# Optimization experiments

Measured on AMD Instinct MI355X. Metric: run time of the kernel, lower is better.

The kernel has to match this reference:

```python
import jax, jax.numpy as jnp
import numpy as np

B, T, D_MODEL, HEAD = 8, 2048, 1024, 64
NEG = -1e9  # finite mask fill; exp underflows to 0 in softmax, avoids inf/NaN


def setup_inputs() -> dict:
    key = jax.random.key(0)
    k1, k2, k3, k4, k5 = jax.random.split(key, 5)
    x = jax.random.normal(k1, (B, T, D_MODEL), dtype=jnp.float32)
    valid_lens = jax.random.randint(k2, (B,), 0, T)
    # nn.Linear(d_model, head_size, bias=False): y = x @ W, W: (d_model, head_size)
    s = 0.02
    Wq = jax.random.normal(k3, (D_MODEL, HEAD), dtype=jnp.float32) * s
    Wk = jax.random.normal(k4, (D_MODEL, HEAD), dtype=jnp.float32) * s
    Wv = jax.random.normal(k5, (D_MODEL, HEAD), dtype=jnp.float32) * s
    return {"x": x, "Wq": Wq, "Wk": Wk, "Wv": Wv, "valid_lens": valid_lens}


def reference(x, Wq, Wk, Wv, valid_lens):
    # x: (B, T, D), projections -> (B, T, H)
    q = jnp.einsum("btd,dh->bth", x, Wq)
    k = jnp.einsum("btd,dh->bth", x, Wk)
    v = jnp.einsum("btd,dh->bth", x, Wv)
    scale = k.shape[-1] ** -0.5
    wei = jnp.einsum("bqh,bkh->bqk", q, k) * scale  # (B, T, T)

    t = jnp.arange(T)
    causal = t[None, :] <= t[:, None]                     # (T, T) lower-tri
    valid = t[None, :] < valid_lens[:, None]              # (B, T)
    mask = causal[None, :, :] & valid[:, :, None] & valid[:, None, :]  # (B, T, T)

    wei = jnp.where(mask, wei, NEG)
    attn = jax.nn.softmax(wei, axis=2)
    # rows with no valid key get all-masked scores -> original code zeros them out
    row_all_masked = ~jnp.any(mask, axis=2)               # (B, T)
    attn = jnp.where(row_all_masked[:, :, None], 0.0, attn)
    # dropout(p=0.0) == identity
    out = jnp.einsum("bqk,bkh->bqh", attn, v)             # (B, T, H)
    return out
```

## Files before the change

kernel.cpp:

```cpp
#include <hip/hip_runtime.h>
#include <hip/hip_bf16.h>
#include <stdint.h>

#define T_   2048
#define DM_  1024
#define HD_  64
#define NROW 16384

typedef __attribute__((ext_vector_type(8))) __bf16 bf16x8;
typedef __attribute__((ext_vector_type(4))) __bf16 bf16x4;
typedef __attribute__((ext_vector_type(4))) float  f32x4;

__global__ void wconv_k(const float* __restrict__ Wq, const float* __restrict__ Wk,
                        const float* __restrict__ Wv, __bf16* __restrict__ wfrag) {
    int tid  = blockIdx.x * 256 + threadIdx.x;
    int lane = tid & 63;
    int t    = (tid >> 6) % 12;
    int kc   = tid / (12 * 64);
    int c = lane & 15, g = lane >> 4;
    int n = t * 16 + c;
    const float* W = (n < 64) ? Wq : (n < 128) ? Wk : Wv;
    int col = n & 63;
    int k0  = kc * 32 + g * 8;
    __bf16* dst = wfrag + (size_t)tid * 8;
#pragma unroll
    for (int j = 0; j < 8; ++j) dst[j] = (__bf16)W[(k0 + j) * HD_ + col];
}

__global__ __launch_bounds__(256) void proj_k(const float* __restrict__ x,
        const __bf16* __restrict__ wfrag, __bf16* __restrict__ Qb,
        __bf16* __restrict__ Kb, __bf16* __restrict__ Vt) {
    int lane = threadIdx.x & 63, wave = threadIdx.x >> 6;
    int ng = blockIdx.x >> 8;
    int rt = blockIdx.x & 255;
    int c = lane & 15, g = lane >> 4;
    int row0 = rt * 64 + wave * 16;
    const float* xp = x + (size_t)(row0 + c) * DM_ + g * 8;
    f32x4 acc[4];
#pragma unroll
    for (int t = 0; t < 4; ++t) acc[t] = (f32x4)0.f;
    for (int kc = 0; kc < 32; ++kc) {
        const f32x4* ap = (const f32x4*)(xp + kc * 32);
        f32x4 a0 = ap[0], a1 = ap[1];
        bf16x8 af;
#pragma unroll
        for (int j = 0; j < 4; ++j) { af[j] = (__bf16)a0[j]; af[j + 4] = (__bf16)a1[j]; }
        const bf16x8* bp = (const bf16x8*)(wfrag + (size_t)kc * 12 * 512) + ng * 256;
#pragma unroll
        for (int t = 0; t < 4; ++t) {
            bf16x8 bf = bp[t * 64 + lane];
            acc[t] = __builtin_amdgcn_mfma_f32_16x16x32_bf16(af, bf, acc[t], 0, 0, 0);
        }
    }
#pragma unroll
    for (int t = 0; t < 4; ++t) {
        int ncol = t * 16 + c;
#pragma unroll
        for (int r = 0; r < 4; ++r) {
            int grow = row0 + g * 4 + r;
            float v  = acc[t][r];
            if (ng == 0)      Qb[(size_t)grow * HD_ + ncol] = (__bf16)(v * 0.125f);
            else if (ng == 1) Kb[(size_t)grow * HD_ + ncol] = (__bf16)v;
            else              Vt[(size_t)(grow >> 11) * (HD_ * T_) + (size_t)ncol * T_ + (grow & 2047)] = (__bf16)v;
        }
    }
}

__global__ __launch_bounds__(128) void attn_k(const __bf16* __restrict__ Qb,
        const __bf16* __restrict__ Kb, const __bf16* __restrict__ Vt,
        const int* __restrict__ vlen, float* __restrict__ out) {
    int bid  = blockIdx.x;
    int half = bid >> 8, idx = bid & 255;
    int b = idx >> 5, p = idx & 31;
    int qb = half ? (63 - p) : p;
    int wave = threadIdx.x >> 6, lane = threadIdx.x & 63;
    int c = lane & 15, g = lane >> 4;
    int qg = qb * 32 + wave * 16 + c;
    const __bf16* qp = Qb + (size_t)(b * T_ + qg) * HD_ + g * 8;
    bf16x8 qf0 = *(const bf16x8*)qp;
    bf16x8 qf1 = *(const bf16x8*)(qp + 32);
    const __bf16* Kbase = Kb + (size_t)b * T_ * HD_;
    const __bf16* Vbase = Vt + (size_t)b * HD_ * T_;
    f32x4 o0 = (f32x4)0.f, o1 = (f32x4)0.f, o2 = (f32x4)0.f, o3 = (f32x4)0.f;
    float m = -1e30f, lsum = 0.f;
    __shared__ __bf16 plds[2][16][72];
    __bf16 (*pl)[72] = plds[wave];
    int nd2 = (qb + 2) >> 1;
    for (int kt = 0; kt < nd2; ++kt) {
        int kv0 = kt * 64;
        const __bf16* kp = Kbase + (size_t)(kv0 + c) * HD_ + g * 8;
        bf16x8 ka00 = *(const bf16x8*)(kp);
        bf16x8 ka01 = *(const bf16x8*)(kp + 32);
        bf16x8 ka10 = *(const bf16x8*)(kp + 16 * HD_);
        bf16x8 ka11 = *(const bf16x8*)(kp + 16 * HD_ + 32);
        bf16x8 kb00 = *(const bf16x8*)(kp + 32 * HD_);
        bf16x8 kb01 = *(const bf16x8*)(kp + 32 * HD_ + 32);
        bf16x8 kb10 = *(const bf16x8*)(kp + 48 * HD_);
        bf16x8 kb11 = *(const bf16x8*)(kp + 48 * HD_ + 32);
        f32x4 sa0 = (f32x4)0.f, sa1 = (f32x4)0.f, sb0 = (f32x4)0.f, sb1 = (f32x4)0.f;
        sa0 = __builtin_amdgcn_mfma_f32_16x16x32_bf16(ka00, qf0, sa0, 0, 0, 0);
        sa0 = __builtin_amdgcn_mfma_f32_16x16x32_bf16(ka01, qf1, sa0, 0, 0, 0);
        sa1 = __builtin_amdgcn_mfma_f32_16x16x32_bf16(ka10, qf0, sa1, 0, 0, 0);
        sa1 = __builtin_amdgcn_mfma_f32_16x16x32_bf16(ka11, qf1, sa1, 0, 0, 0);
        sb0 = __builtin_amdgcn_mfma_f32_16x16x32_bf16(kb00, qf0, sb0, 0, 0, 0);
        sb0 = __builtin_amdgcn_mfma_f32_16x16x32_bf16(kb01, qf1, sb0, 0, 0, 0);
        sb1 = __builtin_amdgcn_mfma_f32_16x16x32_bf16(kb10, qf0, sb1, 0, 0, 0);
        sb1 = __builtin_amdgcn_mfma_f32_16x16x32_bf16(kb11, qf1, sb1, 0, 0, 0);
        float s[16];
#pragma unroll
        for (int r = 0; r < 4; ++r) {
            s[r] = sa0[r]; s[4 + r] = sa1[r]; s[8 + r] = sb0[r]; s[12 + r] = sb1[r];
        }
        if (kt == nd2 - 1) {
#pragma unroll
            for (int i = 0; i < 16; ++i) {
                int kv = kv0 + (i >> 2) * 16 + g * 4 + (i & 3);
                if (kv > qg) s[i] = -1e30f;
            }
        }
        float tm = s[0];
#pragma unroll
        for (int i = 1; i < 16; ++i) tm = fmaxf(tm, s[i]);
        tm = fmaxf(tm, __shfl_xor(tm, 16));
        tm = fmaxf(tm, __shfl_xor(tm, 32));
        float mn = fmaxf(m, tm);
        float al = __expf(m - mn);
        float ps = 0.f;
#pragma unroll
        for (int i = 0; i < 16; ++i) { s[i] = __expf(s[i] - mn); ps += s[i]; }
        ps += __shfl_xor(ps, 16);
        ps += __shfl_xor(ps, 32);
        lsum = lsum * al + ps;
        m = mn;
        o0 *= al; o1 *= al; o2 *= al; o3 *= al;
#pragma unroll
        for (int mt = 0; mt < 4; ++mt) {
            bf16x4 pv;
#pragma unroll
            for (int r = 0; r < 4; ++r) pv[r] = (__bf16)s[mt * 4 + r];
            *(bf16x4*)&pl[c][mt * 16 + g * 4] = pv;
        }
        bf16x8 pf0 = *(const bf16x8*)&pl[c][g * 8];
        bf16x8 pf1 = *(const bf16x8*)&pl[c][32 + g * 8];
        const __bf16* vp = Vbase + (size_t)c * T_ + kv0 + g * 8;
        bf16x8 v0a = *(const bf16x8*)(vp);
        bf16x8 v1a = *(const bf16x8*)(vp + 16 * T_);
        bf16x8 v2a = *(const bf16x8*)(vp + 32 * T_);
        bf16x8 v3a = *(const bf16x8*)(vp + 48 * T_);
        bf16x8 v0b = *(const bf16x8*)(vp + 32);
        bf16x8 v1b = *(const bf16x8*)(vp + 16 * T_ + 32);
        bf16x8 v2b = *(const bf16x8*)(vp + 32 * T_ + 32);
        bf16x8 v3b = *(const bf16x8*)(vp + 48 * T_ + 32);
        o0 = __builtin_amdgcn_mfma_f32_16x16x32_bf16(v0a, pf0, o0, 0, 0, 0);
        o1 = __builtin_amdgcn_mfma_f32_16x16x32_bf16(v1a, pf0, o1, 0, 0, 0);
        o2 = __builtin_amdgcn_mfma_f32_16x16x32_bf16(v2a, pf0, o2, 0, 0, 0);
        o3 = __builtin_amdgcn_mfma_f32_16x16x32_bf16(v3a, pf0, o3, 0, 0, 0);
        o0 = __builtin_amdgcn_mfma_f32_16x16x32_bf16(v0b, pf1, o0, 0, 0, 0);
        o1 = __builtin_amdgcn_mfma_f32_16x16x32_bf16(v1b, pf1, o1, 0, 0, 0);
        o2 = __builtin_amdgcn_mfma_f32_16x16x32_bf16(v2b, pf1, o2, 0, 0, 0);
        o3 = __builtin_amdgcn_mfma_f32_16x16x32_bf16(v3b, pf1, o3, 0, 0, 0);
    }
    float inv  = 1.f / lsum;
    bool  dead = (qg >= vlen[b]);
    float* op  = out + (size_t)(b * T_ + qg) * HD_ + g * 4;
    f32x4 r0 = dead ? (f32x4)0.f : o0 * inv;
    f32x4 r1 = dead ? (f32x4)0.f : o1 * inv;
    f32x4 r2 = dead ? (f32x4)0.f : o2 * inv;
    f32x4 r3 = dead ? (f32x4)0.f : o3 * inv;
    *(f32x4*)(op)      = r0;
    *(f32x4*)(op + 16) = r1;
    *(f32x4*)(op + 32) = r2;
    *(f32x4*)(op + 48) = r3;
}

extern "C" void kernel_launch(void* const* d_in, const int* in_sizes, int n_in,
                              void* d_out, int out_size, void* d_ws, size_t ws_size,
                              hipStream_t stream) {
    const float* x   = (const float*)d_in[0];
    const float* Wq  = (const float*)d_in[1];
    const float* Wk  = (const float*)d_in[2];
    const float* Wv  = (const float*)d_in[3];
    const int*   vln = (const int*)d_in[4];
    float* out = (float*)d_out;

    __bf16* Qb    = (__bf16*)d_ws;
    __bf16* Kb    = Qb + (size_t)NROW * HD_;
    __bf16* Vt    = Kb + (size_t)NROW * HD_;
    __bf16* wfrag = Vt + (size_t)NROW * HD_;

    wconv_k<<<96, 256, 0, stream>>>(Wq, Wk, Wv, wfrag);
    proj_k <<<768, 256, 0, stream>>>(x, wfrag, Qb, Kb, Vt);
    attn_k <<<512, 128, 0, stream>>>(Qb, Kb, Vt, vln, out);
}
```

Baseline: 175.4 us.

## Split attention KV loop four ways and merge partials in a combine kernel

Splits each query tile's causal KV loop into four interleaved partitions run by separate blocks. Each block writes unnormalised partial outputs plus running max and sum to workspace, and a new combine kernel merges them with log-sum-exp rescaling and applies the valid-length zeroing. This raises block count to increase GPU occupancy and parallelism. The softmax also switches to exp2 by folding log2(e) into the Q scale. It adds a second launch and extra float partial traffic through global memory.

```diff
diff --git a/kernel.cpp b/kernel.cpp
--- a/kernel.cpp
+++ b/kernel.cpp
@@ -6,6 +6,7 @@
 #define DM_  1024
 #define HD_  64
 #define NROW 16384
+#define SPLIT 4
 
 typedef __attribute__((ext_vector_type(8))) __bf16 bf16x8;
 typedef __attribute__((ext_vector_type(4))) __bf16 bf16x4;
@@ -59,7 +60,7 @@
         for (int r = 0; r < 4; ++r) {
             int grow = row0 + g * 4 + r;
             float v  = acc[t][r];
-            if (ng == 0)      Qb[(size_t)grow * HD_ + ncol] = (__bf16)(v * 0.125f);
+            if (ng == 0)      Qb[(size_t)grow * HD_ + ncol] = (__bf16)(v * 0.18033688f);
             else if (ng == 1) Kb[(size_t)grow * HD_ + ncol] = (__bf16)v;
             else              Vt[(size_t)(grow >> 11) * (HD_ * T_) + (size_t)ncol * T_ + (grow & 2047)] = (__bf16)v;
         }
@@ -68,109 +69,141 @@
 
 __global__ __launch_bounds__(128) void attn_k(const __bf16* __restrict__ Qb,
         const __bf16* __restrict__ Kb, const __bf16* __restrict__ Vt,
-        const int* __restrict__ vlen, float* __restrict__ out) {
-    int bid  = blockIdx.x;
-    int half = bid >> 8, idx = bid & 255;
+        float* __restrict__ Opart, float* __restrict__ ml) {
+    int split = blockIdx.x >> 9;
+    int bid2  = blockIdx.x & 511;
+    int half = bid2 >> 8, idx = bid2 & 255;
     int b = idx >> 5, p = idx & 31;
     int qb = half ? (63 - p) : p;
     int wave = threadIdx.x >> 6, lane = threadIdx.x & 63;
     int c = lane & 15, g = lane >> 4;
-    int qg = qb * 32 + wave * 16 + c;
-    const __bf16* qp = Qb + (size_t)(b * T_ + qg) * HD_ + g * 8;
-    bf16x8 qf0 = *(const bf16x8*)qp;
-    bf16x8 qf1 = *(const bf16x8*)(qp + 32);
-    const __bf16* Kbase = Kb + (size_t)b * T_ * HD_;
-    const __bf16* Vbase = Vt + (size_t)b * HD_ * T_;
-    f32x4 o0 = (f32x4)0.f, o1 = (f32x4)0.f, o2 = (f32x4)0.f, o3 = (f32x4)0.f;
+    int qg   = qb * 32 + wave * 16 + c;
+    int tile = b * 128 + qb * 2 + wave;
+    int nd2  = (qb + 2) >> 1;
     float m = -1e30f, lsum = 0.f;
-    __shared__ __bf16 plds[2][16][72];
-    __bf16 (*pl)[72] = plds[wave];
-    int nd2 = (qb + 2) >> 1;
-    for (int kt = 0; kt < nd2; ++kt) {
-        int kv0 = kt * 64;
-        const __bf16* kp = Kbase + (size_t)(kv0 + c) * HD_ + g * 8;
-        bf16x8 ka00 = *(const bf16x8*)(kp);
-        bf16x8 ka01 = *(const bf16x8*)(kp + 32);
-        bf16x8 ka10 = *(const bf16x8*)(kp + 16 * HD_);
-        bf16x8 ka11 = *(const bf16x8*)(kp + 16 * HD_ + 32);
-        bf16x8 kb00 = *(const bf16x8*)(kp + 32 * HD_);
-        bf16x8 kb01 = *(const bf16x8*)(kp + 32 * HD_ + 32);
-        bf16x8 kb10 = *(const bf16x8*)(kp + 48 * HD_);
-        bf16x8 kb11 = *(const bf16x8*)(kp + 48 * HD_ + 32);
-        f32x4 sa0 = (f32x4)0.f, sa1 = (f32x4)0.f, sb0 = (f32x4)0.f, sb1 = (f32x4)0.f;
-        sa0 = __builtin_amdgcn_mfma_f32_16x16x32_bf16(ka00, qf0, sa0, 0, 0, 0);
-        sa0 = __builtin_amdgcn_mfma_f32_16x16x32_bf16(ka01, qf1, sa0, 0, 0, 0);
-        sa1 = __builtin_amdgcn_mfma_f32_16x16x32_bf16(ka10, qf0, sa1, 0, 0, 0);
-        sa1 = __builtin_amdgcn_mfma_f32_16x16x32_bf16(ka11, qf1, sa1, 0, 0, 0);
-        sb0 = __builtin_amdgcn_mfma_f32_16x16x32_bf16(kb00, qf0, sb0, 0, 0, 0);
-        sb0 = __builtin_amdgcn_mfma_f32_16x16x32_bf16(kb01, qf1, sb0, 0, 0, 0);
-        sb1 = __builtin_amdgcn_mfma_f32_16x16x32_bf16(kb10, qf0, sb1, 0, 0, 0);
-        sb1 = __builtin_amdgcn_mfma_f32_16x16x32_bf16(kb11, qf1, sb1, 0, 0, 0);
-        float s[16];
-#pragma unroll
-        for (int r = 0; r < 4; ++r) {
-            s[r] = sa0[r]; s[4 + r] = sa1[r]; s[8 + r] = sb0[r]; s[12 + r] = sb1[r];
-        }
-        if (kt == nd2 - 1) {
-#pragma unroll
-            for (int i = 0; i < 16; ++i) {
-                int kv = kv0 + (i >> 2) * 16 + g * 4 + (i & 3);
-                if (kv > qg) s[i] = -1e30f;
+    if (split < nd2) {
+        const __bf16* qp = Qb + (size_t)(b * T_ + qg) * HD_ + g * 8;
+        bf16x8 qf0 = *(const bf16x8*)qp;
+        bf16x8 qf1 = *(const bf16x8*)(qp + 32);
+        const __bf16* Kbase = Kb + (size_t)b * T_ * HD_;
+        const __bf16* Vbase = Vt + (size_t)b * HD_ * T_;
+        f32x4 o0 = (f32x4)0.f, o1 = (f32x4)0.f, o2 = (f32x4)0.f, o3 = (f32x4)0.f;
+        __shared__ __bf16 plds[2][16][72];
+        __bf16 (*pl)[72] = plds[wave];
+        for (int kt = split; kt < nd2; kt += SPLIT) {
+            int kv0 = kt * 64;
+            const __bf16* kp = Kbase + (size_t)(kv0 + c) * HD_ + g * 8;
+            bf16x8 ka00 = *(const bf16x8*)(kp);
+            bf16x8 ka01 = *(const bf16x8*)(kp + 32);
+            bf16x8 ka10 = *(const bf16x8*)(kp + 16 * HD_);
+            bf16x8 ka11 = *(const bf16x8*)(kp + 16 * HD_ + 32);
+            bf16x8 kb00 = *(const bf16x8*)(kp + 32 * HD_);
+            bf16x8 kb01 = *(const bf16x8*)(kp + 32 * HD_ + 32);
+            bf16x8 kb10 = *(const bf16x8*)(kp + 48 * HD_);
+            bf16x8 kb11 = *(const bf16x8*)(kp + 48 * HD_ + 32);
+            f32x4 sa0 = (f32x4)0.f, sa1 = (f32x4)0.f, sb0 = (f32x4)0.f, sb1 = (f32x4)0.f;
+            sa0 = __builtin_amdgcn_mfma_f32_16x16x32_bf16(ka00, qf0, sa0, 0, 0, 0);
+            sa0 = __builtin_amdgcn_mfma_f32_16x16x32_bf16(ka01, qf1, sa0, 0, 0, 0);
+            sa1 = __builtin_amdgcn_mfma_f32_16x16x32_bf16(ka10, qf0, sa1, 0, 0, 0);
+            sa1 = __builtin_amdgcn_mfma_f32_16x16x32_bf16(ka11, qf1, sa1, 0, 0, 0);
+            sb0 = __builtin_amdgcn_mfma_f32_16x16x32_bf16(kb00, qf0, sb0, 0, 0, 0);
+            sb0 = __builtin_amdgcn_mfma_f32_16x16x32_bf16(kb01, qf1, sb0, 0, 0, 0);
+            sb1 = __builtin_amdgcn_mfma_f32_16x16x32_bf16(kb10, qf0, sb1, 0, 0, 0);
+            sb1 = __builtin_amdgcn_mfma_f32_16x16x32_bf16(kb11, qf1, sb1, 0, 0, 0);
+            float s[16];
+#pragma unroll
+            for (int r = 0; r < 4; ++r) {
+                s[r] = sa0[r]; s[4 + r] = sa1[r]; s[8 + r] = sb0[r]; s[12 + r] = sb1[r];
             }
-        }
-        float tm = s[0];
-#pragma unroll
-        for (int i = 1; i < 16; ++i) tm = fmaxf(tm, s[i]);
-        tm = fmaxf(tm, __shfl_xor(tm, 16));
-        tm = fmaxf(tm, __shfl_xor(tm, 32));
-        float mn = fmaxf(m, tm);
-        float al = __expf(m - mn);
-        float ps = 0.f;
-#pragma unroll
-        for (int i = 0; i < 16; ++i) { s[i] = __expf(s[i] - mn); ps += s[i]; }
-        ps += __shfl_xor(ps, 16);
-        ps += __shfl_xor(ps, 32);
-        lsum = lsum * al + ps;
-        m = mn;
-        o0 *= al; o1 *= al; o2 *= al; o3 *= al;
-#pragma unroll
-        for (int mt = 0; mt < 4; ++mt) {
-            bf16x4 pv;
-#pragma unroll
-            for (int r = 0; r < 4; ++r) pv[r] = (__bf16)s[mt * 4 + r];
-            *(bf16x4*)&pl[c][mt * 16 + g * 4] = pv;
-        }
-        bf16x8 pf0 = *(const bf16x8*)&pl[c][g * 8];
-        bf16x8 pf1 = *(const bf16x8*)&pl[c][32 + g * 8];
-        const __bf16* vp = Vbase + (size_t)c * T_ + kv0 + g * 8;
-        bf16x8 v0a = *(const bf16x8*)(vp);
-        bf16x8 v1a = *(const bf16x8*)(vp + 16 * T_);
-        bf16x8 v2a = *(const bf16x8*)(vp + 32 * T_);
-        bf16x8 v3a = *(const bf16x8*)(vp + 48 * T_);
-        bf16x8 v0b = *(const bf16x8*)(vp + 32);
-        bf16x8 v1b = *(const bf16x8*)(vp + 16 * T_ + 32);
-        bf16x8 v2b = *(const bf16x8*)(vp + 32 * T_ + 32);
-        bf16x8 v3b = *(const bf16x8*)(vp + 48 * T_ + 32);
-        o0 = __builtin_amdgcn_mfma_f32_16x16x32_bf16(v0a, pf0, o0, 0, 0, 0);
-        o1 = __builtin_amdgcn_mfma_f32_16x16x32_bf16(v1a, pf0, o1, 0, 0, 0);
-        o2 = __builtin_amdgcn_mfma_f32_16x16x32_bf16(v2a, pf0, o2, 0, 0, 0);
-        o3 = __builtin_amdgcn_mfma_f32_16x16x32_bf16(v3a, pf0, o3, 0, 0, 0);
-        o0 = __builtin_amdgcn_mfma_f32_16x16x32_bf16(v0b, pf1, o0, 0, 0, 0);
-        o1 = __builtin_amdgcn_mfma_f32_16x16x32_bf16(v1b, pf1, o1, 0, 0, 0);
-        o2 = __builtin_amdgcn_mfma_f32_16x16x32_bf16(v2b, pf1, o2, 0, 0, 0);
-        o3 = __builtin_amdgcn_mfma_f32_16x16x32_bf16(v3b, pf1, o3, 0, 0, 0);
-    }
-    float inv  = 1.f / lsum;
-    bool  dead = (qg >= vlen[b]);
-    float* op  = out + (size_t)(b * T_ + qg) * HD_ + g * 4;
-    f32x4 r0 = dead ? (f32x4)0.f : o0 * inv;
-    f32x4 r1 = dead ? (f32x4)0.f : o1 * inv;
-    f32x4 r2 = dead ? (f32x4)0.f : o2 * inv;
-    f32x4 r3 = dead ? (f32x4)0.f : o3 * inv;
-    *(f32x4*)(op)      = r0;
-    *(f32x4*)(op + 16) = r1;
-    *(f32x4*)(op + 32) = r2;
-    *(f32x4*)(op + 48) = r3;
+            if (kt == nd2 - 1) {
+#pragma unroll
+                for (int i = 0; i < 16; ++i) {
+                    int kv = kv0 + (i >> 2) * 16 + g * 4 + (i & 3);
+                    if (kv > qg) s[i] = -1e30f;
+                }
+            }
+            float tm = s[0];
+#pragma unroll
+            for (int i = 1; i < 16; ++i) tm = fmaxf(tm, s[i]);
+            tm = fmaxf(tm, __shfl_xor(tm, 16));
+            tm = fmaxf(tm, __shfl_xor(tm, 32));
+            float mn = fmaxf(m, tm);
+            float al = __builtin_amdgcn_exp2f(m - mn);
+            float ps = 0.f;
+#pragma unroll
+            for (int i = 0; i < 16; ++i) { s[i] = __builtin_amdgcn_exp2f(s[i] - mn); ps += s[i]; }
+            ps += __shfl_xor(ps, 16);
+            ps += __shfl_xor(ps, 32);
+            lsum = lsum * al + ps;
+            m = mn;
+            o0 *= al; o1 *= al; o2 *= al; o3 *= al;
+#pragma unroll
+            for (int mt = 0; mt < 4; ++mt) {
+                bf16x4 pv;
+#pragma unroll
+                for (int r = 0; r < 4; ++r) pv[r] = (__bf16)s[mt * 4 + r];
+                *(bf16x4*)&pl[c][mt * 16 + g * 4] = pv;
+            }
+            bf16x8 pf0 = *(const bf16x8*)&pl[c][g * 8];
+            bf16x8 pf1 = *(const bf16x8*)&pl[c][32 + g * 8];
+            const __bf16* vp = Vbase + (size_t)c * T_ + kv0 + g * 8;
+            bf16x8 v0a = *(const bf16x8*)(vp);
+            bf16x8 v1a = *(const bf16x8*)(vp + 16 * T_);
+            bf16x8 v2a = *(const bf16x8*)(vp + 32 * T_);
+            bf16x8 v3a = *(const bf16x8*)(vp + 48 * T_);
+            bf16x8 v0b = *(const bf16x8*)(vp + 32);
+            bf16x8 v1b = *(const bf16x8*)(vp + 16 * T_ + 32);
+            bf16x8 v2b = *(const bf16x8*)(vp + 32 * T_ + 32);
+            bf16x8 v3b = *(const bf16x8*)(vp + 48 * T_ + 32);
+            o0 = __builtin_amdgcn_mfma_f32_16x16x32_bf16(v0a, pf0, o0, 0, 0, 0);
+            o1 = __builtin_amdgcn_mfma_f32_16x16x32_bf16(v1a, pf0, o1, 0, 0, 0);
+            o2 = __builtin_amdgcn_mfma_f32_16x16x32_bf16(v2a, pf0, o2, 0, 0, 0);
+            o3 = __builtin_amdgcn_mfma_f32_16x16x32_bf16(v3a, pf0, o3, 0, 0, 0);
+            o0 = __builtin_amdgcn_mfma_f32_16x16x32_bf16(v0b, pf1, o0, 0, 0, 0);
+            o1 = __builtin_amdgcn_mfma_f32_16x16x32_bf16(v1b, pf1, o1, 0, 0, 0);
+            o2 = __builtin_amdgcn_mfma_f32_16x16x32_bf16(v2b, pf1, o2, 0, 0, 0);
+            o3 = __builtin_amdgcn_mfma_f32_16x16x32_bf16(v3b, pf1, o3, 0, 0, 0);
+        }
+        float* op = Opart + ((size_t)tile * SPLIT + split) * 1024 + c * 64 + g * 4;
+        *(f32x4*)(op)      = o0;
+        *(f32x4*)(op + 16) = o1;
+        *(f32x4*)(op + 32) = o2;
+        *(f32x4*)(op + 48) = o3;
+    }
+    if (g == 0) {
+        float* mlp = ml + ((size_t)tile * SPLIT + split) * 32 + c * 2;
+        mlp[0] = m; mlp[1] = lsum;
+    }
+}
+
+__global__ __launch_bounds__(256) void comb_k(const float* __restrict__ Opart,
+        const float* __restrict__ ml, const int* __restrict__ vlen,
+        float* __restrict__ out) {
+    int tile = blockIdx.x;
+    int b  = tile >> 7;
+    int q0 = (tile & 127) * 16;
+    int q  = threadIdx.x >> 4;
+    int d0 = (threadIdx.x & 15) * 4;
+    int qg = q0 + q;
+    const float* mlp = ml + (size_t)tile * SPLIT * 32 + q * 2;
+    float mj[SPLIT], lj[SPLIT];
+#pragma unroll
+    for (int j = 0; j < SPLIT; ++j) { mj[j] = mlp[j * 32]; lj[j] = mlp[j * 32 + 1]; }
+    float M = fmaxf(fmaxf(mj[0], mj[1]), fmaxf(mj[2], mj[3]));
+    f32x4 acc = (f32x4)0.f;
+    float L = 0.f;
+#pragma unroll
+    for (int j = 0; j < SPLIT; ++j) {
+        if (lj[j] > 0.f) {
+            float sc = __builtin_amdgcn_exp2f(mj[j] - M);
+            L += lj[j] * sc;
+            f32x4 ov = *(const f32x4*)(Opart + ((size_t)tile * SPLIT + j) * 1024 + q * 64 + d0);
+            acc += ov * sc;
+        }
+    }
+    float inv = (qg < vlen[b]) ? 1.f / L : 0.f;
+    f32x4 r = acc * inv;
+    *(f32x4*)(out + ((size_t)(b * T_) + qg) * HD_ + d0) = r;
 }
 
 extern "C" void kernel_launch(void* const* d_in, const int* in_sizes, int n_in,
@@ -187,8 +220,11 @@
     __bf16* Kb    = Qb + (size_t)NROW * HD_;
     __bf16* Vt    = Kb + (size_t)NROW * HD_;
     __bf16* wfrag = Vt + (size_t)NROW * HD_;
+    float*  Opart = (float*)(wfrag + 24576 * 8);
+    float*  mlbuf = Opart + (size_t)1024 * SPLIT * 1024;
 
     wconv_k<<<96, 256, 0, stream>>>(Wq, Wk, Wv, wfrag);
     proj_k <<<768, 256, 0, stream>>>(x, wfrag, Qb, Kb, Vt);
-    attn_k <<<512, 128, 0, stream>>>(Qb, Kb, Vt, vln, out);
-}
+    attn_k <<<512 * SPLIT, 128, 0, stream>>>(Qb, Kb, Vt, Opart, mlbuf);
+    comb_k <<<1024, 256, 0, stream>>>(Opart, mlbuf, vln, out);
+}
```

Measured after the change: 170.5 us. -2.8%, faster.
